# Optimization experiments

Measured on AMD Instinct MI355X. Metric: run time of the kernel, lower is better.

Reference implementation:

```python
import jax, jax.numpy as jnp
import numpy as np

N_NODES = 50000
N_EDGES = 800000
D = 96
L = 4
N_GRAPHS = 256
BN_EPS = 1e-5


def setup_inputs() -> dict:
    key = jax.random.key(0)
    ks = jax.random.split(key, 8)
    x = jax.random.normal(ks[0], (N_NODES, D), dtype=jnp.float32)
    edge_index = jax.random.randint(ks[1], (2, N_EDGES), 0, N_NODES, dtype=jnp.int32)
    batch = jnp.sort(jax.random.randint(ks[2], (N_NODES,), 0, N_GRAPHS, dtype=jnp.int32))
    # Stacked per-layer parameters (all layers are 96->96).
    W = jax.random.normal(ks[3], (L, D, D), dtype=jnp.float32) / np.sqrt(D)
    b = jnp.zeros((L, D), dtype=jnp.float32)
    gamma = jnp.ones((L, D), dtype=jnp.float32)
    beta = jnp.zeros((L, D), dtype=jnp.float32)
    return {"x": x, "edge_index": edge_index, "batch": batch,
            "W": W, "b": b, "gamma": gamma, "beta": beta}


def _gcn_norm(edge_index):
    # Add self loops and compute symmetric normalization (PyG gcn_norm).
    loops = jnp.arange(N_NODES, dtype=edge_index.dtype)
    src = jnp.concatenate([edge_index[0], loops])  # [E+N]
    dst = jnp.concatenate([edge_index[1], loops])
    deg = jax.ops.segment_sum(jnp.ones_like(dst, dtype=jnp.float32), dst,
                              num_segments=N_NODES)
    dis = jnp.where(deg > 0, jax.lax.rsqrt(jnp.maximum(deg, 1.0)), 0.0)
    norm = dis[src] * dis[dst]  # [E+N]
    return src, dst, norm


def reference(x, edge_index, batch, W, b, gamma, beta):
    src, dst, norm = _gcn_norm(edge_index)
    h = x
    for i in range(L):
        # GCNConv: linear transform, then normalized scatter-add aggregation.
        hw = h @ W[i]                                  # [N, D]
        agg = jax.ops.segment_sum(hw[src] * norm[:, None], dst,
                                  num_segments=N_NODES) + b[i]
        # BatchNorm1d over nodes (training-mode batch statistics, biased var).
        mu = jnp.mean(agg, axis=0)
        var = jnp.mean(jnp.square(agg - mu), axis=0)
        hn = (agg - mu) * jax.lax.rsqrt(var + BN_EPS) * gamma[i] + beta[i]
        h = jax.nn.relu(hn)
        # dropout is identity in eval / deterministic reference
    # global_mean_pool
    sums = jax.ops.segment_sum(h, batch, num_segments=N_GRAPHS)     # [G, D]
    cnt = jax.ops.segment_sum(jnp.ones((N_NODES,), jnp.float32), batch,
                              num_segments=N_GRAPHS)
    return sums / jnp.maximum(cnt, 1.0)[:, None]
```

## Files before the change

### kernel.cpp

```cpp
#include <hip/hip_runtime.h>
#include <hip/hip_bf16.h>
#include <hip/hip_fp16.h>

#define N_NODES 50000
#define N_EDGES 800000
#define DD 96
#define NLAYER 4
#define N_GRAPHS 256
#define BN_EPS 1e-5f
#define SLABS 8
#define SFEAT 12
#define GSU 8
#define NCHUNK 64
#define CHUNK_E (N_EDGES / NCHUNK)
#define NRANGE 4
#define RANGE_N 12544

typedef _Float16 half8_t __attribute__((ext_vector_type(8)));
typedef float floatx4 __attribute__((ext_vector_type(4)));

enum : size_t {
  O_CNT    = 0,
  O_STATS  = O_CNT + N_NODES,
  O_POOL   = O_STATS + 4 * 192,
  O_GCNT   = O_POOL + N_GRAPHS * DD,
  ZERO_END = O_GCNT + N_GRAPHS,
  O_ROWPTR = ZERO_END,
  O_DIS    = O_ROWPTR + N_NODES + 1,
  O_BSUMS  = O_DIS + N_NODES,
  O_EDGE   = (O_BSUMS + 256 + 7) & ~size_t(7),
  O_HWH    = (O_EDGE + N_EDGES + 7) & ~size_t(7),
  O_PART   = O_HWH + (size_t)SLABS * N_NODES * GSU,
  O_LOCC   = O_PART + (size_t)NCHUNK * N_NODES / 2,
  O_P      = O_LOCC + N_EDGES / 2,
  WS_ELEMS = O_P + (size_t)N_NODES * DD
};

__device__ __forceinline__ void atomAddF(float* p, float v) {
  unsafeAtomicAdd(p, v);
}

__device__ __forceinline__ float2 h2f(unsigned int u) {
  __half2 h = *(__half2*)&u;
  return __half22float2(h);
}

__global__ __launch_bounds__(256) void k_phist(const int* __restrict__ dst,
                                               unsigned short* __restrict__ part,
                                               unsigned short* __restrict__ locc) {
  __shared__ int hist[RANGE_N];
  const int b = blockIdx.x;
  const int tid = threadIdx.x;
  const int e0 = b * CHUNK_E, e1 = e0 + CHUNK_E;
  for (int r = 0; r < NRANGE; ++r) {
    const int r0 = r * RANGE_N;
    for (int i = tid; i < RANGE_N; i += 256) hist[i] = 0;
    __syncthreads();
    for (int e = e0 + tid; e < e1; e += 256) {
      unsigned rel = (unsigned)(dst[e] - r0);
      if (rel < RANGE_N) locc[e] = (unsigned short)atomicAdd(&hist[rel], 1);
    }
    __syncthreads();
    for (int i = tid; i < RANGE_N; i += 256) {
      int n = r0 + i;
      if (n < N_NODES) part[(size_t)b * N_NODES + n] = (unsigned short)hist[i];
    }
    __syncthreads();
  }
}

__global__ __launch_bounds__(256) void k_reduce(unsigned short* __restrict__ part,
                                                int* __restrict__ cnt,
                                                float* __restrict__ dis,
                                                int* __restrict__ bsums) {
  __shared__ int s[256];
  const int tid = threadIdx.x;
  const int n = blockIdx.x * 256 + tid;
  int run = 0;
  if (n < N_NODES) {
#pragma unroll 8
    for (int b = 0; b < NCHUNK; ++b) {
      size_t idx = (size_t)b * N_NODES + n;
      int t = part[idx];
      part[idx] = (unsigned short)run;
      run += t;
    }
    cnt[n] = run;
    dis[n] = rsqrtf((float)(run + 1));
  }
  s[tid] = (n < N_NODES) ? run : 0;
  __syncthreads();
  for (int off = 128; off > 0; off >>= 1) {
    if (tid < off) s[tid] += s[tid + off];
    __syncthreads();
  }
  if (tid == 0) bsums[blockIdx.x] = s[0];
}

__device__ __forceinline__ int lbound(const int* __restrict__ a, int v) {
  int lo = 0, hi = N_NODES;
  while (lo < hi) { int m = (lo + hi) >> 1; if (a[m] < v) lo = m + 1; else hi = m; }
  return lo;
}

__global__ __launch_bounds__(256) void k_scan_bsums(int* __restrict__ bsums, int nb,
                                                    int* __restrict__ rowptr,
                                                    const int* __restrict__ batch,
                                                    int* __restrict__ gcnt) {
  __shared__ int s[256];
  int tid = threadIdx.x;
  int v = (tid < nb) ? bsums[tid] : 0;
  s[tid] = v;
  __syncthreads();
  for (int off = 1; off < 256; off <<= 1) {
    int add = (tid >= off) ? s[tid - off] : 0;
    __syncthreads();
    s[tid] += add;
    __syncthreads();
  }
  if (tid < nb) bsums[tid] = s[tid] - v;
  if (tid == 255) rowptr[N_NODES] = s[255];
  gcnt[tid] = lbound(batch, tid + 1) - lbound(batch, tid);
}

__global__ __launch_bounds__(256) void k_scan_write(const int* __restrict__ cnt,
                                                    const int* __restrict__ bsums,
                                                    int* __restrict__ rowptr) {
  __shared__ int s[256];
  int i = blockIdx.x * 256 + threadIdx.x;
  int v = (i < N_NODES) ? cnt[i] : 0;
  s[threadIdx.x] = v;
  __syncthreads();
  for (int off = 1; off < 256; off <<= 1) {
    int x = 0;
    if (threadIdx.x >= off) x = s[threadIdx.x - off];
    __syncthreads();
    s[threadIdx.x] += x;
    __syncthreads();
  }
  if (i < N_NODES) rowptr[i] = bsums[blockIdx.x] + s[threadIdx.x] - v;
}

__global__ __launch_bounds__(256) void k_fill(const int* __restrict__ ei,
                                              const int* __restrict__ rowptr,
                                              const unsigned short* __restrict__ part,
                                              const unsigned short* __restrict__ locc,
                                              const float* __restrict__ dis,
                                              unsigned int* __restrict__ edg) {
  int e = blockIdx.x * 256 + threadIdx.x;
  if (e >= N_EDGES) return;
  int s = ei[e];
  int d = ei[N_EDGES + e];
  int chunk = e / CHUNK_E;
  int pos = rowptr[d] + (int)part[(size_t)chunk * N_NODES + d] + (int)locc[e];
  unsigned short wb = __half_as_ushort(__float2half_rn(dis[s] * dis[d]));
  edg[pos] = (unsigned int)s | ((unsigned int)wb << 16);
}

__global__ __launch_bounds__(256) void k_gemm(const float* __restrict__ X,
                                              const float* __restrict__ Wg,
                                              const float* __restrict__ stats,
                                              const float* __restrict__ gamma,
                                              const float* __restrict__ beta,
                                              unsigned int* __restrict__ Yu) {
  __shared__ _Float16 Xh[64 * 104];
  __shared__ _Float16 Wt[96 * 104];
  __shared__ float sA[96], sC[96];
  const int tid = threadIdx.x;
  const int row0 = blockIdx.x * 64;

  if (tid < 96) {
    if (stats) {
      float mu = stats[tid] * (1.f / N_NODES);
      float var = fmaxf(stats[96 + tid] * (1.f / N_NODES) - mu * mu, 0.f);
      float a = gamma[tid] * rsqrtf(var + BN_EPS);
      sA[tid] = a;
      sC[tid] = beta[tid] - mu * a;
    } else {
      sA[tid] = 1.f;
      sC[tid] = 0.f;
    }
  }
  for (int i = tid; i < 96 * 24; i += 256) {
    int n = i / 24, k0 = (i % 24) * 4;
    union { _Float16 h[4]; uint2 u; } pk;
    pk.h[0] = (_Float16)Wg[(k0 + 0) * 96 + n];
    pk.h[1] = (_Float16)Wg[(k0 + 1) * 96 + n];
    pk.h[2] = (_Float16)Wg[(k0 + 2) * 96 + n];
    pk.h[3] = (_Float16)Wg[(k0 + 3) * 96 + n];
    *(uint2*)&Wt[n * 104 + k0] = pk.u;
  }
  __syncthreads();
  const bool bn = (stats != nullptr);
  for (int i = tid; i < 64 * 24; i += 256) {
    int r = i / 24, c4 = (i % 24) * 4;
    int gr = row0 + r;
    float4 v = (gr < N_NODES) ? *(const float4*)&X[(size_t)gr * 96 + c4]
                              : make_float4(0.f, 0.f, 0.f, 0.f);
    if (bn) {
      v.x = fmaxf(v.x * sA[c4] + sC[c4], 0.f);
      v.y = fmaxf(v.y * sA[c4 + 1] + sC[c4 + 1], 0.f);
      v.z = fmaxf(v.z * sA[c4 + 2] + sC[c4 + 2], 0.f);
      v.w = fmaxf(v.w * sA[c4 + 3] + sC[c4 + 3], 0.f);
    }
    union { _Float16 h[4]; uint2 u; } pk;
    pk.h[0] = (_Float16)v.x; pk.h[1] = (_Float16)v.y;
    pk.h[2] = (_Float16)v.z; pk.h[3] = (_Float16)v.w;
    *(uint2*)&Xh[r * 104 + c4] = pk.u;
  }
  __syncthreads();

  const int w = tid >> 6, lane = tid & 63;
  const int quad = lane >> 4, l16 = lane & 15;

  half8_t a[3];
#pragma unroll
  for (int kb = 0; kb < 3; ++kb)
    a[kb] = *(const half8_t*)&Xh[(w * 16 + l16) * 104 + kb * 32 + quad * 8];

  floatx4 acc[6];
#pragma unroll
  for (int nt = 0; nt < 6; ++nt) acc[nt] = (floatx4){0.f, 0.f, 0.f, 0.f};
#pragma unroll
  for (int nt = 0; nt < 6; ++nt) {
#pragma unroll
    for (int kb = 0; kb < 3; ++kb) {
      half8_t b = *(const half8_t*)&Wt[(nt * 16 + l16) * 104 + kb * 32 + quad * 8];
      acc[nt] = __builtin_amdgcn_mfma_f32_16x16x32_f16(a[kb], b, acc[nt], 0, 0, 0);
    }
  }

  __syncthreads();
#pragma unroll
  for (int nt = 0; nt < 6; ++nt) {
#pragma unroll
    for (int reg = 0; reg < 4; ++reg) {
      int r = w * 16 + quad * 4 + reg;
      Xh[r * 104 + nt * 16 + l16] = (_Float16)acc[nt][reg];
    }
  }
  __syncthreads();
  for (int i = tid; i < 64 * 24; i += 256) {
    int r = i / 24, rem = i % 24;
    int slab = rem / 3, up = rem % 3;
    int node = row0 + r;
    if (node < N_NODES) {
      uint2 u = *(const uint2*)&Xh[r * 104 + slab * SFEAT + up * 4];
      *(uint2*)&Yu[((size_t)slab * N_NODES + node) * GSU + up * 2] = u;
    }
  }
}

__global__ __launch_bounds__(256) void k_gather(const unsigned int* __restrict__ hw4,
                                                const int* __restrict__ rowptr,
                                                const unsigned int* __restrict__ edg,
                                                const float* __restrict__ dis,
                                                float* __restrict__ agg,
                                                float* __restrict__ stats) {
  __shared__ float sred[24];
  const int tid = threadIdx.x;
  const int slab = blockIdx.x & (SLABS - 1);
  const int chunk = blockIdx.x >> 3;
  const int wave = tid >> 6;
  const int lane = tid & 63;
  const int g = lane / 6;
  const int ch = lane - g * 6;
  const int n = chunk * 40 + wave * 10 + g;
  const bool valid = (g < 10) && (n < N_NODES);
  const int nc = valid ? n : 0;

  const unsigned int* slabU = hw4 + (size_t)slab * N_NODES * GSU;

  if (tid < 24) sred[tid] = 0.f;

  const int js = valid ? rowptr[nc] : 0;
  const int je = valid ? rowptr[nc + 1] : 0;

  float a0 = 0.f, a1 = 0.f;
  if (valid) {
    float dn = dis[nc];
    float s2 = dn * dn;
    float2 f = h2f(slabU[nc * GSU + ch]);
    a0 = f.x * s2;
    a1 = f.y * s2;
  }

  for (int j = js; j < je; j += 8) {
    unsigned int ew[8];
    unsigned int rv[8];
#pragma unroll
    for (int k = 0; k < 8; ++k) {
      int jk = j + k;
      int jc = jk < je ? jk : (je - 1);
      ew[k] = edg[jc];
    }
#pragma unroll
    for (int k = 0; k < 8; ++k)
      rv[k] = slabU[(size_t)(ew[k] & 0xFFFFu) * GSU + ch];
#pragma unroll
    for (int k = 0; k < 8; ++k) {
      float w = (j + k < je)
                    ? __half2float(__ushort_as_half((unsigned short)(ew[k] >> 16)))
                    : 0.f;
      float2 f = h2f(rv[k]);
      a0 = fmaf(w, f.x, a0);
      a1 = fmaf(w, f.y, a1);
    }
  }

  if (valid) {
    *(float2*)&agg[(size_t)n * DD + slab * SFEAT + ch * 2] = make_float2(a0, a1);
  }

  __syncthreads();
  if (valid) {
    atomicAdd(&sred[ch * 2], a0);
    atomicAdd(&sred[ch * 2 + 1], a1);
    atomicAdd(&sred[12 + ch * 2], a0 * a0);
    atomicAdd(&sred[13 + ch * 2], a1 * a1);
  }
  __syncthreads();
  if (tid < 24) {
    int c = (tid < 12) ? (slab * SFEAT + tid) : (96 + slab * SFEAT + tid - 12);
    atomAddF(&stats[c], sred[tid]);
  }
}

__global__ __launch_bounds__(192) void k_pool(const float* __restrict__ h,
                                              const float* __restrict__ stats,
                                              const float* __restrict__ gamma,
                                              const float* __restrict__ beta,
                                              const int* __restrict__ batch,
                                              float* __restrict__ pool) {
  __shared__ float sA[96], sC[96];
  const int tid = threadIdx.x;
  if (tid < 96) {
    float mu = stats[tid] * (1.f / N_NODES);
    float var = fmaxf(stats[96 + tid] * (1.f / N_NODES) - mu * mu, 0.f);
    float a = gamma[tid] * rsqrtf(var + BN_EPS);
    sA[tid] = a;
    sC[tid] = beta[tid] - mu * a;
  }
  __syncthreads();
  const int chain = blockIdx.x * 8 + tid / 24;
  const int q4 = (tid % 24) * 4;
  int n0 = chain * 32;
  if (n0 >= N_NODES) return;
  int n1 = min(n0 + 32, N_NODES);
  float A0 = sA[q4], A1 = sA[q4 + 1], A2 = sA[q4 + 2], A3 = sA[q4 + 3];
  float C0 = sC[q4], C1 = sC[q4 + 1], C2 = sC[q4 + 2], C3 = sC[q4 + 3];
  int cur = batch[n0];
  float4 acc = make_float4(0.f, 0.f, 0.f, 0.f);
  for (int n = n0; n < n1; ++n) {
    int g = batch[n];
    if (g != cur) {
      float* p = &pool[cur * 96 + q4];
      atomAddF(p, acc.x); atomAddF(p + 1, acc.y);
      atomAddF(p + 2, acc.z); atomAddF(p + 3, acc.w);
      acc = make_float4(0.f, 0.f, 0.f, 0.f);
      cur = g;
    }
    const float4 v = *(const float4*)&h[(size_t)n * 96 + q4];
    acc.x += fmaxf(v.x * A0 + C0, 0.f);
    acc.y += fmaxf(v.y * A1 + C1, 0.f);
    acc.z += fmaxf(v.z * A2 + C2, 0.f);
    acc.w += fmaxf(v.w * A3 + C3, 0.f);
  }
  float* p = &pool[cur * 96 + q4];
  atomAddF(p, acc.x); atomAddF(p + 1, acc.y);
  atomAddF(p + 2, acc.z); atomAddF(p + 3, acc.w);
}

__global__ void k_out(const float* __restrict__ pool, const int* __restrict__ gcnt,
                      float* __restrict__ out) {
  int t = blockIdx.x * blockDim.x + threadIdx.x;
  if (t >= N_GRAPHS * 96) return;
  int g = t / 96;
  int c = gcnt[g];
  if (c < 1) c = 1;
  out[t] = pool[t] / (float)c;
}

extern "C" void kernel_launch(void* const* d_in, const int* in_sizes, int n_in,
                              void* d_out, int out_size, void* d_ws, size_t ws_size,
                              hipStream_t stream) {
  const float* x     = (const float*)d_in[0];
  const int*   ei    = (const int*)d_in[1];
  const int*   batch = (const int*)d_in[2];
  const float* W     = (const float*)d_in[3];
  const float* gamma = (const float*)d_in[5];
  const float* beta  = (const float*)d_in[6];
  float* out = (float*)d_out;

  float* ws = (float*)d_ws;
  int*   cnt    = (int*)(ws + O_CNT);
  float* stats  = ws + O_STATS;
  float* pool   = ws + O_POOL;
  int*   gcnt   = (int*)(ws + O_GCNT);
  int*   rowptr = (int*)(ws + O_ROWPTR);
  float* dis    = ws + O_DIS;
  int*   bsums  = (int*)(ws + O_BSUMS);
  unsigned int* edg = (unsigned int*)(ws + O_EDGE);
  unsigned int* hw4 = (unsigned int*)(ws + O_HWH);
  unsigned short* part = (unsigned short*)(ws + O_PART);
  unsigned short* locc = (unsigned short*)(ws + O_LOCC);
  float* P      = ws + O_P;

  hipMemsetAsync(stats, 0, (ZERO_END - O_STATS) * sizeof(float), stream);

  const int eb = (N_EDGES + 255) / 256;
  const int nb = (N_NODES + 255) / 256;
  k_phist<<<NCHUNK, 256, 0, stream>>>(ei + N_EDGES, part, locc);
  k_reduce<<<nb, 256, 0, stream>>>(part, cnt, dis, bsums);
  k_scan_bsums<<<1, 256, 0, stream>>>(bsums, nb, rowptr, batch, gcnt);
  k_scan_write<<<nb, 256, 0, stream>>>(cnt, bsums, rowptr);
  k_fill<<<eb, 256, 0, stream>>>(ei, rowptr, part, locc, dis, edg);

  const int gemmb = (N_NODES + 63) / 64;
  const int gatherb = SLABS * ((N_NODES + 39) / 40);

  const float* hin = x;
  for (int l = 0; l < NLAYER; ++l) {
    const float* st = (l == 0) ? nullptr : (stats + (l - 1) * 192);
    const float* ga = (l == 0) ? nullptr : (gamma + (l - 1) * 96);
    const float* be = (l == 0) ? nullptr : (beta + (l - 1) * 96);
    k_gemm<<<gemmb, 256, 0, stream>>>(hin, W + l * 96 * 96, st, ga, be, hw4);
    k_gather<<<gatherb, 256, 0, stream>>>(hw4, rowptr, edg, dis, P, stats + l * 192);
    hin = P;
  }

  const int poolb = ((N_NODES + 31) / 32 + 7) / 8;
  k_pool<<<poolb, 192, 0, stream>>>(P, stats + 3 * 192, gamma + 3 * 96, beta + 3 * 96,
                                    batch, pool);
  k_out<<<(N_GRAPHS * 96 + 255) / 256, 256, 0, stream>>>(pool, gcnt, out);
}
```

Measured before the change: 576.1 us.

## Sort nodes by in-degree for balanced gather and precompute fp16 weights once

Builds a counting-sort permutation of nodes keyed by in-degree (capped at 255), using per-block degree histograms, a global scan and a scatter kernel. The gather kernel then processes nodes in that order so lanes within a wave have similar edge counts, which is meant to cut divergence and idle lanes in the variable-length edge loop. Separately, the transposed fp16 weights for all layers are built once in k_reduce, and each GEMM block copies them with vector loads instead of re-converting per block. The cost is an extra kernel, extra setup work, and gather writes and self-loads that now follow permuted, less sequential node order.

```diff
diff --git a/kernel.cpp b/kernel.cpp
--- a/kernel.cpp
+++ b/kernel.cpp
@@ -15,6 +15,7 @@
 #define CHUNK_E (N_EDGES / NCHUNK)
 #define NRANGE 4
 #define RANGE_N 12544
+#define NB_NODE 196
 
 typedef _Float16 half8_t __attribute__((ext_vector_type(8)));
 typedef float floatx4 __attribute__((ext_vector_type(4)));
@@ -28,7 +29,10 @@
   O_ROWPTR = ZERO_END,
   O_DIS    = O_ROWPTR + N_NODES + 1,
   O_BSUMS  = O_DIS + N_NODES,
-  O_EDGE   = (O_BSUMS + 256 + 7) & ~size_t(7),
+  O_PERM   = O_BSUMS + 256,
+  O_DPART  = O_PERM + N_NODES,
+  O_W16    = O_DPART + NB_NODE * 256 / 2,
+  O_EDGE   = (O_W16 + 4 * 96 * 104 / 2 + 7) & ~size_t(7),
   O_HWH    = (O_EDGE + N_EDGES + 7) & ~size_t(7),
   O_PART   = O_HWH + (size_t)SLABS * N_NODES * GSU,
   O_LOCC   = O_PART + (size_t)NCHUNK * N_NODES / 2,
@@ -72,10 +76,30 @@
 __global__ __launch_bounds__(256) void k_reduce(unsigned short* __restrict__ part,
                                                 int* __restrict__ cnt,
                                                 float* __restrict__ dis,
-                                                int* __restrict__ bsums) {
+                                                int* __restrict__ bsums,
+                                                unsigned short* __restrict__ dpart,
+                                                const float* __restrict__ Wg,
+                                                _Float16* __restrict__ W16) {
   __shared__ int s[256];
+  __shared__ int dh[256];
   const int tid = threadIdx.x;
   const int n = blockIdx.x * 256 + tid;
+  dh[tid] = 0;
+  {
+    const int gt = blockIdx.x * 256 + tid;
+    const int items = 4 * 96 * 24;
+    for (int i = gt; i < items; i += NB_NODE * 256) {
+      int l = i / (96 * 24), rem = i % (96 * 24);
+      int nn = rem / 24, k0 = (rem % 24) * 4;
+      const float* wl = Wg + (size_t)l * 96 * 96;
+      union { _Float16 h[4]; uint2 u; } pk;
+      pk.h[0] = (_Float16)wl[(k0 + 0) * 96 + nn];
+      pk.h[1] = (_Float16)wl[(k0 + 1) * 96 + nn];
+      pk.h[2] = (_Float16)wl[(k0 + 2) * 96 + nn];
+      pk.h[3] = (_Float16)wl[(k0 + 3) * 96 + nn];
+      *(uint2*)&W16[((size_t)l * 96 + nn) * 104 + k0] = pk.u;
+    }
+  }
   int run = 0;
   if (n < N_NODES) {
 #pragma unroll 8
@@ -88,8 +112,11 @@
     cnt[n] = run;
     dis[n] = rsqrtf((float)(run + 1));
   }
+  __syncthreads();
+  if (n < N_NODES) atomicAdd(&dh[min(run, 255)], 1);
   s[tid] = (n < N_NODES) ? run : 0;
   __syncthreads();
+  dpart[blockIdx.x * 256 + tid] = (unsigned short)dh[tid];
   for (int off = 128; off > 0; off >>= 1) {
     if (tid < off) s[tid] += s[tid + off];
     __syncthreads();
@@ -106,8 +133,10 @@
 __global__ __launch_bounds__(256) void k_scan_bsums(int* __restrict__ bsums, int nb,
                                                     int* __restrict__ rowptr,
                                                     const int* __restrict__ batch,
-                                                    int* __restrict__ gcnt) {
+                                                    int* __restrict__ gcnt,
+                                                    unsigned short* __restrict__ dpart) {
   __shared__ int s[256];
+  __shared__ int sb[256];
   int tid = threadIdx.x;
   int v = (tid < nb) ? bsums[tid] : 0;
   s[tid] = v;
@@ -121,6 +150,24 @@
   if (tid < nb) bsums[tid] = s[tid] - v;
   if (tid == 255) rowptr[N_NODES] = s[255];
   gcnt[tid] = lbound(batch, tid + 1) - lbound(batch, tid);
+  int run = 0;
+  for (int b = 0; b < NB_NODE; ++b) {
+    int t = dpart[b * 256 + tid];
+    dpart[b * 256 + tid] = (unsigned short)run;
+    run += t;
+  }
+  sb[tid] = run;
+  __syncthreads();
+  int mysum = run;
+  for (int off = 1; off < 256; off <<= 1) {
+    int add = (tid >= off) ? sb[tid - off] : 0;
+    __syncthreads();
+    sb[tid] += add;
+    __syncthreads();
+  }
+  int binstart = sb[tid] - mysum;
+  for (int b = 0; b < NB_NODE; ++b)
+    dpart[b * 256 + tid] = (unsigned short)(dpart[b * 256 + tid] + binstart);
 }
 
 __global__ __launch_bounds__(256) void k_scan_write(const int* __restrict__ cnt,
@@ -139,6 +186,21 @@
     __syncthreads();
   }
   if (i < N_NODES) rowptr[i] = bsums[blockIdx.x] + s[threadIdx.x] - v;
+}
+
+__global__ __launch_bounds__(256) void k_scatter(const int* __restrict__ cnt,
+                                                 const unsigned short* __restrict__ dpart,
+                                                 int* __restrict__ perm) {
+  __shared__ int h[256];
+  const int tid = threadIdx.x;
+  h[tid] = 0;
+  __syncthreads();
+  const int n = blockIdx.x * 256 + tid;
+  if (n < N_NODES) {
+    int bin = min(cnt[n], 255);
+    int r = atomicAdd(&h[bin], 1);
+    perm[(int)dpart[blockIdx.x * 256 + bin] + r] = n;
+  }
 }
 
 __global__ __launch_bounds__(256) void k_fill(const int* __restrict__ ei,
@@ -158,7 +220,7 @@
 }
 
 __global__ __launch_bounds__(256) void k_gemm(const float* __restrict__ X,
-                                              const float* __restrict__ Wg,
+                                              const _Float16* __restrict__ Wh16,
                                               const float* __restrict__ stats,
                                               const float* __restrict__ gamma,
                                               const float* __restrict__ beta,
@@ -181,15 +243,8 @@
       sC[tid] = 0.f;
     }
   }
-  for (int i = tid; i < 96 * 24; i += 256) {
-    int n = i / 24, k0 = (i % 24) * 4;
-    union { _Float16 h[4]; uint2 u; } pk;
-    pk.h[0] = (_Float16)Wg[(k0 + 0) * 96 + n];
-    pk.h[1] = (_Float16)Wg[(k0 + 1) * 96 + n];
-    pk.h[2] = (_Float16)Wg[(k0 + 2) * 96 + n];
-    pk.h[3] = (_Float16)Wg[(k0 + 3) * 96 + n];
-    *(uint2*)&Wt[n * 104 + k0] = pk.u;
-  }
+  for (int i = tid; i < 96 * 104 / 8; i += 256)
+    *(uint4*)&Wt[i * 8] = *(const uint4*)&Wh16[i * 8];
   __syncthreads();
   const bool bn = (stats != nullptr);
   for (int i = tid; i < 64 * 24; i += 256) {
@@ -255,6 +310,7 @@
                                                 const int* __restrict__ rowptr,
                                                 const unsigned int* __restrict__ edg,
                                                 const float* __restrict__ dis,
+                                                const int* __restrict__ perm,
                                                 float* __restrict__ agg,
                                                 float* __restrict__ stats) {
   __shared__ float sred[24];
@@ -265,9 +321,9 @@
   const int lane = tid & 63;
   const int g = lane / 6;
   const int ch = lane - g * 6;
-  const int n = chunk * 40 + wave * 10 + g;
-  const bool valid = (g < 10) && (n < N_NODES);
-  const int nc = valid ? n : 0;
+  const int idx = chunk * 40 + wave * 10 + g;
+  const bool valid = (g < 10) && (idx < N_NODES);
+  const int nc = valid ? perm[idx] : 0;
 
   const unsigned int* slabU = hw4 + (size_t)slab * N_NODES * GSU;
 
@@ -280,7 +336,7 @@
   if (valid) {
     float dn = dis[nc];
     float s2 = dn * dn;
-    float2 f = h2f(slabU[nc * GSU + ch]);
+    float2 f = h2f(slabU[(size_t)nc * GSU + ch]);
     a0 = f.x * s2;
     a1 = f.y * s2;
   }
@@ -309,7 +365,7 @@
   }
 
   if (valid) {
-    *(float2*)&agg[(size_t)n * DD + slab * SFEAT + ch * 2] = make_float2(a0, a1);
+    *(float2*)&agg[(size_t)nc * DD + slab * SFEAT + ch * 2] = make_float2(a0, a1);
   }
 
   __syncthreads();
@@ -400,6 +456,9 @@
   int*   rowptr = (int*)(ws + O_ROWPTR);
   float* dis    = ws + O_DIS;
   int*   bsums  = (int*)(ws + O_BSUMS);
+  int*   perm   = (int*)(ws + O_PERM);
+  unsigned short* dpart = (unsigned short*)(ws + O_DPART);
+  _Float16* W16 = (_Float16*)(ws + O_W16);
   unsigned int* edg = (unsigned int*)(ws + O_EDGE);
   unsigned int* hw4 = (unsigned int*)(ws + O_HWH);
   unsigned short* part = (unsigned short*)(ws + O_PART);
@@ -409,11 +468,11 @@
   hipMemsetAsync(stats, 0, (ZERO_END - O_STATS) * sizeof(float), stream);
 
   const int eb = (N_EDGES + 255) / 256;
-  const int nb = (N_NODES + 255) / 256;
   k_phist<<<NCHUNK, 256, 0, stream>>>(ei + N_EDGES, part, locc);
-  k_reduce<<<nb, 256, 0, stream>>>(part, cnt, dis, bsums);
-  k_scan_bsums<<<1, 256, 0, stream>>>(bsums, nb, rowptr, batch, gcnt);
-  k_scan_write<<<nb, 256, 0, stream>>>(cnt, bsums, rowptr);
+  k_reduce<<<NB_NODE, 256, 0, stream>>>(part, cnt, dis, bsums, dpart, W, W16);
+  k_scan_bsums<<<1, 256, 0, stream>>>(bsums, NB_NODE, rowptr, batch, gcnt, dpart);
+  k_scan_write<<<NB_NODE, 256, 0, stream>>>(cnt, bsums, rowptr);
+  k_scatter<<<NB_NODE, 256, 0, stream>>>(cnt, dpart, perm);
   k_fill<<<eb, 256, 0, stream>>>(ei, rowptr, part, locc, dis, edg);
 
   const int gemmb = (N_NODES + 63) / 64;
@@ -424,8 +483,9 @@
     const float* st = (l == 0) ? nullptr : (stats + (l - 1) * 192);
     const float* ga = (l == 0) ? nullptr : (gamma + (l - 1) * 96);
     const float* be = (l == 0) ? nullptr : (beta + (l - 1) * 96);
-    k_gemm<<<gemmb, 256, 0, stream>>>(hin, W + l * 96 * 96, st, ga, be, hw4);
-    k_gather<<<gatherb, 256, 0, stream>>>(hw4, rowptr, edg, dis, P, stats + l * 192);
+    k_gemm<<<gemmb, 256, 0, stream>>>(hin, W16 + (size_t)l * 96 * 104, st, ga, be, hw4);
+    k_gather<<<gatherb, 256, 0, stream>>>(hw4, rowptr, edg, dis, perm, P,
+                                          stats + l * 192);
     hin = P;
   }
 
```

Measured after the change: 591.2 us. 1.03x slower.

## Pack histogram counters and precompute fp16 transposed weights once

Applied to the files above, without the earlier changes.

The degree histogram kernel now loads each chunk's destination indices into registers once. It packs two 16-bit counters per shared int, which cuts the range passes from four to two. Separately, the weight transpose and fp16 conversion move out of every GEMM block into the reduce kernel, so each GEMM block only does a vectorized copy of pre-packed weights. The costs are high register use for 49 held indices and possible 16-bit counter overflow if a node gets more than 65535 edges in one chunk.

```diff
diff --git a/kernel.cpp b/kernel.cpp
--- a/kernel.cpp
+++ b/kernel.cpp
@@ -13,8 +13,11 @@
 #define GSU 8
 #define NCHUNK 64
 #define CHUNK_E (N_EDGES / NCHUNK)
-#define NRANGE 4
-#define RANGE_N 12544
+#define NB_NODE 196
+#define PH_RANGES 2
+#define PH_RN 25000
+#define PH_HI 12500
+#define PH_NE 49
 
 typedef _Float16 half8_t __attribute__((ext_vector_type(8)));
 typedef float floatx4 __attribute__((ext_vector_type(4)));
@@ -28,7 +31,8 @@
   O_ROWPTR = ZERO_END,
   O_DIS    = O_ROWPTR + N_NODES + 1,
   O_BSUMS  = O_DIS + N_NODES,
-  O_EDGE   = (O_BSUMS + 256 + 7) & ~size_t(7),
+  O_W16    = O_BSUMS + 256,
+  O_EDGE   = (O_W16 + 4 * 96 * 104 / 2 + 7) & ~size_t(7),
   O_HWH    = (O_EDGE + N_EDGES + 7) & ~size_t(7),
   O_PART   = O_HWH + (size_t)SLABS * N_NODES * GSU,
   O_LOCC   = O_PART + (size_t)NCHUNK * N_NODES / 2,
@@ -48,22 +52,35 @@
 __global__ __launch_bounds__(256) void k_phist(const int* __restrict__ dst,
                                                unsigned short* __restrict__ part,
                                                unsigned short* __restrict__ locc) {
-  __shared__ int hist[RANGE_N];
-  const int b = blockIdx.x;
-  const int tid = threadIdx.x;
-  const int e0 = b * CHUNK_E, e1 = e0 + CHUNK_E;
-  for (int r = 0; r < NRANGE; ++r) {
-    const int r0 = r * RANGE_N;
-    for (int i = tid; i < RANGE_N; i += 256) hist[i] = 0;
-    __syncthreads();
-    for (int e = e0 + tid; e < e1; e += 256) {
-      unsigned rel = (unsigned)(dst[e] - r0);
-      if (rel < RANGE_N) locc[e] = (unsigned short)atomicAdd(&hist[rel], 1);
-    }
-    __syncthreads();
-    for (int i = tid; i < RANGE_N; i += 256) {
-      int n = r0 + i;
-      if (n < N_NODES) part[(size_t)b * N_NODES + n] = (unsigned short)hist[i];
+  __shared__ int hist[PH_HI];
+  const int b = blockIdx.x, tid = threadIdx.x;
+  const int e0 = b * CHUNK_E;
+  int regs[PH_NE];
+#pragma unroll
+  for (int i = 0; i < PH_NE; ++i) {
+    int e = e0 + tid + i * 256;
+    regs[i] = (tid + i * 256 < CHUNK_E) ? dst[e] : -1;
+  }
+#pragma unroll
+  for (int r = 0; r < PH_RANGES; ++r) {
+    const int r0 = r * PH_RN;
+    for (int i = tid; i < PH_HI; i += 256) hist[i] = 0;
+    __syncthreads();
+#pragma unroll
+    for (int i = 0; i < PH_NE; ++i) {
+      unsigned rel = (unsigned)(regs[i] - r0);
+      if (rel < PH_RN) {
+        int add = (rel & 1) ? (1 << 16) : 1;
+        int old = atomicAdd(&hist[rel >> 1], add);
+        locc[e0 + tid + i * 256] =
+            (unsigned short)((rel & 1) ? (old >> 16) : (old & 0xFFFF));
+      }
+    }
+    __syncthreads();
+    for (int i = tid; i < PH_RN; i += 256) {
+      int v = hist[i >> 1];
+      part[(size_t)b * N_NODES + r0 + i] =
+          (unsigned short)((i & 1) ? (v >> 16) : (v & 0xFFFF));
     }
     __syncthreads();
   }
@@ -72,10 +89,27 @@
 __global__ __launch_bounds__(256) void k_reduce(unsigned short* __restrict__ part,
                                                 int* __restrict__ cnt,
                                                 float* __restrict__ dis,
-                                                int* __restrict__ bsums) {
+                                                int* __restrict__ bsums,
+                                                const float* __restrict__ Wg,
+                                                _Float16* __restrict__ W16) {
   __shared__ int s[256];
   const int tid = threadIdx.x;
   const int n = blockIdx.x * 256 + tid;
+  {
+    const int gt = blockIdx.x * 256 + tid;
+    const int items = 4 * 96 * 24;
+    for (int i = gt; i < items; i += NB_NODE * 256) {
+      int l = i / (96 * 24), rem = i % (96 * 24);
+      int nn = rem / 24, k0 = (rem % 24) * 4;
+      const float* wl = Wg + (size_t)l * 96 * 96;
+      union { _Float16 h[4]; uint2 u; } pk;
+      pk.h[0] = (_Float16)wl[(k0 + 0) * 96 + nn];
+      pk.h[1] = (_Float16)wl[(k0 + 1) * 96 + nn];
+      pk.h[2] = (_Float16)wl[(k0 + 2) * 96 + nn];
+      pk.h[3] = (_Float16)wl[(k0 + 3) * 96 + nn];
+      *(uint2*)&W16[((size_t)l * 96 + nn) * 104 + k0] = pk.u;
+    }
+  }
   int run = 0;
   if (n < N_NODES) {
 #pragma unroll 8
@@ -158,7 +192,7 @@
 }
 
 __global__ __launch_bounds__(256) void k_gemm(const float* __restrict__ X,
-                                              const float* __restrict__ Wg,
+                                              const _Float16* __restrict__ Wh16,
                                               const float* __restrict__ stats,
                                               const float* __restrict__ gamma,
                                               const float* __restrict__ beta,
@@ -181,15 +215,8 @@
       sC[tid] = 0.f;
     }
   }
-  for (int i = tid; i < 96 * 24; i += 256) {
-    int n = i / 24, k0 = (i % 24) * 4;
-    union { _Float16 h[4]; uint2 u; } pk;
-    pk.h[0] = (_Float16)Wg[(k0 + 0) * 96 + n];
-    pk.h[1] = (_Float16)Wg[(k0 + 1) * 96 + n];
-    pk.h[2] = (_Float16)Wg[(k0 + 2) * 96 + n];
-    pk.h[3] = (_Float16)Wg[(k0 + 3) * 96 + n];
-    *(uint2*)&Wt[n * 104 + k0] = pk.u;
-  }
+  for (int i = tid; i < 96 * 104 / 8; i += 256)
+    *(uint4*)&Wt[i * 8] = *(const uint4*)&Wh16[i * 8];
   __syncthreads();
   const bool bn = (stats != nullptr);
   for (int i = tid; i < 64 * 24; i += 256) {
@@ -280,7 +307,7 @@
   if (valid) {
     float dn = dis[nc];
     float s2 = dn * dn;
-    float2 f = h2f(slabU[nc * GSU + ch]);
+    float2 f = h2f(slabU[(size_t)nc * GSU + ch]);
     a0 = f.x * s2;
     a1 = f.y * s2;
   }
@@ -400,6 +427,7 @@
   int*   rowptr = (int*)(ws + O_ROWPTR);
   float* dis    = ws + O_DIS;
   int*   bsums  = (int*)(ws + O_BSUMS);
+  _Float16* W16 = (_Float16*)(ws + O_W16);
   unsigned int* edg = (unsigned int*)(ws + O_EDGE);
   unsigned int* hw4 = (unsigned int*)(ws + O_HWH);
   unsigned short* part = (unsigned short*)(ws + O_PART);
@@ -409,11 +437,10 @@
   hipMemsetAsync(stats, 0, (ZERO_END - O_STATS) * sizeof(float), stream);
 
   const int eb = (N_EDGES + 255) / 256;
-  const int nb = (N_NODES + 255) / 256;
   k_phist<<<NCHUNK, 256, 0, stream>>>(ei + N_EDGES, part, locc);
-  k_reduce<<<nb, 256, 0, stream>>>(part, cnt, dis, bsums);
-  k_scan_bsums<<<1, 256, 0, stream>>>(bsums, nb, rowptr, batch, gcnt);
-  k_scan_write<<<nb, 256, 0, stream>>>(cnt, bsums, rowptr);
+  k_reduce<<<NB_NODE, 256, 0, stream>>>(part, cnt, dis, bsums, W, W16);
+  k_scan_bsums<<<1, 256, 0, stream>>>(bsums, NB_NODE, rowptr, batch, gcnt);
+  k_scan_write<<<NB_NODE, 256, 0, stream>>>(cnt, bsums, rowptr);
   k_fill<<<eb, 256, 0, stream>>>(ei, rowptr, part, locc, dis, edg);
 
   const int gemmb = (N_NODES + 63) / 64;
@@ -424,7 +451,7 @@
     const float* st = (l == 0) ? nullptr : (stats + (l - 1) * 192);
     const float* ga = (l == 0) ? nullptr : (gamma + (l - 1) * 96);
     const float* be = (l == 0) ? nullptr : (beta + (l - 1) * 96);
-    k_gemm<<<gemmb, 256, 0, stream>>>(hin, W + l * 96 * 96, st, ga, be, hw4);
+    k_gemm<<<gemmb, 256, 0, stream>>>(hin, W16 + (size_t)l * 96 * 104, st, ga, be, hw4);
     k_gather<<<gatherb, 256, 0, stream>>>(hw4, rowptr, edg, dis, P, stats + l * 192);
     hin = P;
   }
```

After: 498.0 us. 13.6% less time.
